# Optimization experiments

Measured on AMD Instinct MI355X. Metric: run time of the kernel, lower is better.

The kernel has to match this reference:

```python
import jax, jax.numpy as jnp
import numpy as np

B, N, M = 64, 128, 64
LH, LO, LI2, LI3, LI4 = 128, 128, 64, 32, 16


def _celu(x):
    return jax.nn.celu(x, alpha=0.1)


def setup_inputs() -> dict:
    key = jax.random.key(0)
    ks = jax.random.split(key, 32)
    inp = {
        'ai': jax.random.normal(ks[0], (B, N, 3), jnp.float32),
        'aj': jax.random.normal(ks[1], (B, N, M, 3), jnp.float32),
        'ak': jax.random.normal(ks[2], (B, N, M, 3), jnp.float32),
        'al': jax.random.normal(ks[3], (B, N, M, 3), jnp.float32),
    }
    def lin(k, fan_out, fan_in):
        kw, kb = jax.random.split(k)
        s = 1.0 / np.sqrt(fan_in)
        return (jax.random.uniform(kw, (fan_out, fan_in), jnp.float32, -s, s),
                jax.random.uniform(kb, (fan_out,), jnp.float32, -s, s))
    names = ['Wi1', 'Wi2', 'Wj1', 'Wj2', 'Wk1', 'Wk2', 'Wl1', 'Wl2']
    dims = [(LH, 3), (LO, LH)] * 4
    for i, (nm, (fo, fi)) in enumerate(zip(names, dims)):
        W, b = lin(ks[4 + i], fo, fi)
        inp[nm] = W
        inp['b' + nm[1:]] = b
    for i, (nm, (fo, fi)) in enumerate(zip(['W1', 'W2', 'W3', 'W4'],
                                           [(LI2, LO), (LI3, LI2), (LI4, LI3), (1, LI4)])):
        W, b = lin(ks[20 + i], fo, fi)
        inp[nm] = W
        inp['b' + nm[1:]] = b
    return inp


def _mlp2(x, W1, b1, W2, b2):
    return _celu(_celu(x @ W1.T + b1) @ W2.T + b2)


def _pad_mask(x):
    # 0 where the descriptor sums exactly to zero (padding), else 1
    s = x.sum(axis=-1)
    return (s != 0).astype(x.dtype)[..., None]


def reference(ai, aj, ak, al,
              Wi1, bi1, Wi2, bi2, Wj1, bj1, Wj2, bj2,
              Wk1, bk1, Wk2, bk2, Wl1, bl1, Wl2, bl2,
              W1, b1, W2, b2, W3, b3, W4, b4):
    ai_mask = _pad_mask(ai)          # [B,N,1]
    aj_mask = _pad_mask(aj)          # [B,N,M,1]
    ak_mask = _pad_mask(ak)
    al_mask = _pad_mask(al)

    hi = _mlp2(ai, Wi1, bi1, Wi2, bi2) * ai_mask            # [B,N,LO]
    hj = _mlp2(aj, Wj1, bj1, Wj2, bj2) * aj_mask            # [B,N,M,LO]
    hk = _mlp2(ak, Wk1, bk1, Wk2, bk2) * ak_mask
    hl = _mlp2(al, Wl1, bl1, Wl2, bl2) * al_mask

    atm = hi + hj.sum(axis=2) + hk.sum(axis=2) + hl.sum(axis=2)  # [B,N,LO]
    atm = _celu(atm @ W1.T + b1)
    atm = _celu(atm @ W2.T + b2)
    atm = _celu(atm @ W3.T + b3)
    atm = atm @ W4.T + b4                                    # [B,N,1]
    return atm * ai_mask
```

## Files before the change

### kernel.cpp

```cpp
#include <hip/hip_runtime.h>


typedef __attribute__((ext_vector_type(8))) short short8;
typedef __attribute__((ext_vector_type(4))) float f32x4;
typedef __attribute__((ext_vector_type(4))) unsigned uint4v;

#define G_ 8
#define NATOMS (64 * 128)
#define SCL   14.42695040888963f
#define SCL01 1.442695040888963f
#define INVS  0.06931471805599453f

#define LDS_BYTES 39712

struct DartParams {
  const float* x[4];
  const float* W1[4];
  const float* b1[4];
  const float* W2[4];
  const float* b2[4];
  const float* HW[4];
  const float* Hb[4];
  float* out;
};

__device__ __forceinline__ float celu01(float z) {
  float t = fmaf(0.1f, __builtin_amdgcn_exp2f(z * SCL), -0.1f);
  return __builtin_amdgcn_fmed3f(z, t, 0.0f);
}

__device__ __forceinline__ float celu_s(float zs) {
  float t = fmaf(SCL01, __builtin_amdgcn_exp2f(zs), -SCL01);
  return __builtin_amdgcn_fmed3f(zs, t, 0.0f);
}

__device__ __forceinline__ unsigned cvtpk(float a, float b) {
  unsigned r;
  asm("v_cvt_pk_bf16_f32 %0, %1, %2" : "=v"(r) : "v"(a), "v"(b));
  return r;
}
__device__ __forceinline__ short8 pack4(unsigned a, unsigned b, unsigned c, unsigned d) {
  uint4v u = {a, b, c, d};
  return __builtin_bit_cast(short8, u);
}

__device__ __forceinline__ void stage_species(
    const float* W1g, const float* b1g, const float* W2g, const float* b2g,
    f32x4* sW1v, float* sB2v, short8* sBfv,
    int t, int lane, int lq, int lr, int wave) {
  __syncthreads();
  if (t < 128) {
    const float* w = W1g + t * 3;
    f32x4 v;
    v.x = w[0] * SCL; v.y = w[1] * SCL; v.z = w[2] * SCL; v.w = b1g[t] * SCL;
    sW1v[t + (t >> 3)] = v;
    sB2v[t] = b2g[t] * SCL;
  }
#pragma unroll
  for (int ff = 0; ff < 8; ++ff) {
    const int f  = wave * 8 + ff;
    const int ob = f >> 2, kb = f & 3;
    const f32x4* src = (const f32x4*)(W2g + (ob * 16 + lr) * 128 + kb * 32 + lq * 8);
    f32x4 lo = src[0], hi = src[1];
    sBfv[f * 64 + lane] = pack4(cvtpk(lo.x, lo.y), cvtpk(lo.z, lo.w),
                                cvtpk(hi.x, hi.y), cvtpk(hi.z, hi.w));
  }
  __syncthreads();
}

extern "C" __global__ __launch_bounds__(256, 4)
void dart_fused(DartParams p) {
  __shared__ __align__(16) char lds[LDS_BYTES];
  short8* sBfv = (short8*)lds;
  f32x4*  sW1v = (f32x4*)(lds + 32768);
  float*  sB2v = (float*)(lds + 35072);
  float*  sAtm = (float*)(lds + 35584);
  float*  sIm  = (float*)(lds + 39680);
  float*  sH1  = (float*)lds;
  float*  sH2  = (float*)(lds + 2048);
  float*  sH3  = (float*)(lds + 3072);

  const int t    = threadIdx.x;
  const int lane = t & 63;
  const int wave = t >> 6;
  const int lq   = lane >> 4;
  const int lr   = lane & 15;
  const int atom0 = (int)blockIdx.x * G_;

  for (int i = t; i < G_ * 128; i += 256) sAtm[i] = 0.0f;

#pragma unroll 1
  for (int s = 0; s < 3; ++s) {
    stage_species(p.W1[s], p.b1[s], p.W2[s], p.b2[s],
                  sW1v, sB2v, sBfv, t, lane, lq, lr, wave);

    const float* X = p.x[s];
    const int rowoff = wave * 16 + lr;

#pragma unroll 1
    for (int qq = 0; qq < 2; ++qq) {
      const int gq = qq * 4;
      float x0[4], x1[4], x2[4];
#pragma unroll
      for (int a = 0; a < 4; ++a) {
        const float* xp = X + ((atom0 + gq + a) * 64 + rowoff) * 3;
        x0[a] = xp[0]; x1[a] = xp[1]; x2[a] = xp[2];
      }
      float mr[4][4];
#pragma unroll
      for (int a = 0; a < 4; ++a) {
        const unsigned mw = (unsigned)__ballot((x0[a] + x1[a] + x2[a]) != 0.0f);
#pragma unroll
        for (int j = 0; j < 4; ++j)
          mr[a][j] = ((mw >> (lq * 4 + j)) & 1u) ? INVS : 0.0f;
      }

      short8 af[4][4];
#pragma unroll
      for (int kb = 0; kb < 4; ++kb) {
        const f32x4* wrow = sW1v + kb * 36 + lq * 9;
        unsigned u[4][4];
#pragma unroll
        for (int e2 = 0; e2 < 4; ++e2) {
          f32x4 wA = wrow[2 * e2], wB = wrow[2 * e2 + 1];
#pragma unroll
          for (int a = 0; a < 4; ++a) {
            float zA = celu_s(fmaf(x0[a], wA.x, fmaf(x1[a], wA.y, fmaf(x2[a], wA.z, wA.w))));
            float zB = celu_s(fmaf(x0[a], wB.x, fmaf(x1[a], wB.y, fmaf(x2[a], wB.z, wB.w))));
            u[a][e2] = cvtpk(zA, zB);
          }
        }
#pragma unroll
        for (int a = 0; a < 4; ++a)
          af[a][kb] = pack4(u[a][0], u[a][1], u[a][2], u[a][3]);
      }

#pragma unroll
      for (int ob = 0; ob < 8; ++ob) {
        const short8* fb = sBfv + (ob * 4) * 64 + lane;
        const float bv = sB2v[ob * 16 + lr];
        f32x4 ac[4];
#pragma unroll
        for (int a = 0; a < 4; ++a) ac[a] = {bv, bv, bv, bv};
#pragma unroll
        for (int kb = 0; kb < 4; ++kb) {
          short8 fr = fb[kb * 64];
#pragma unroll
          for (int a = 0; a < 4; ++a)
            ac[a] = __builtin_amdgcn_mfma_f32_16x16x32_bf16(af[a][kb], fr, ac[a], 0, 0, 0);
        }
        const int col = ob * 16 + lr;
#pragma unroll
        for (int a = 0; a < 4; ++a) {
          float pa = 0.0f;
#pragma unroll
          for (int j = 0; j < 4; ++j)
            pa = fmaf(celu_s(ac[a][j]), mr[a][j], pa);
          pa += __shfl_xor(pa, 16, 64);
          pa += __shfl_xor(pa, 32, 64);
          if (lane < 16) atomicAdd(&sAtm[(gq + a) * 128 + col], pa);
        }
      }
    }
  }

  {
    stage_species(p.W1[3], p.b1[3], p.W2[3], p.b2[3],
                  sW1v, sB2v, sBfv, t, lane, lq, lr, wave);

    const int ri = min(atom0 + lr, NATOMS - 1);
    const float* xp = p.x[3] + ri * 3;
    const float x0 = xp[0], x1 = xp[1], x2 = xp[2];
    const unsigned mbi = (unsigned)__ballot((x0 + x1 + x2) != 0.0f);

    short8 af[4];
#pragma unroll
    for (int kb = 0; kb < 4; ++kb) {
      const f32x4* wrow = sW1v + kb * 36 + lq * 9;
      unsigned u[4];
#pragma unroll
      for (int e2 = 0; e2 < 4; ++e2) {
        f32x4 wA = wrow[2 * e2], wB = wrow[2 * e2 + 1];
        float cA = celu_s(fmaf(x0, wA.x, fmaf(x1, wA.y, fmaf(x2, wA.z, wA.w))));
        float cB = celu_s(fmaf(x0, wB.x, fmaf(x1, wB.y, fmaf(x2, wB.z, wB.w))));
        u[e2] = cvtpk(cA, cB);
      }
      af[kb] = pack4(u[0], u[1], u[2], u[3]);
    }
#pragma unroll
    for (int oo = 0; oo < 2; ++oo) {
      const int ob = wave * 2 + oo;
      const int col = ob * 16 + lr;
      const float bv = sB2v[col];
      const short8* fb = sBfv + (ob * 4) * 64 + lane;
      f32x4 a = {bv, bv, bv, bv};
#pragma unroll
      for (int kb = 0; kb < 4; ++kb)
        a = __builtin_amdgcn_mfma_f32_16x16x32_bf16(af[kb], fb[kb * 64], a, 0, 0, 0);
#pragma unroll
      for (int j = 0; j < 4; ++j) {
        const int g = lq * 4 + j;
        if (g < G_) {
          float m = ((mbi >> g) & 1u) ? INVS : 0.0f;
          sAtm[g * 128 + col] += celu_s(a[j]) * m;
        }
      }
    }
    if (wave == 0 && t < G_) sIm[t] = (float)((mbi >> t) & 1u);
    __syncthreads();
  }

  {
    const int g = t >> 4, u = t & 15;
    const bool act = (g < G_);
    if (act) {
      const f32x4* atm4 = (const f32x4*)(sAtm + g * 128);
#pragma unroll
      for (int rep = 0; rep < 4; ++rep) {
        const int o = rep * 16 + u;
        const f32x4* w4 = (const f32x4*)(p.HW[0] + o * 128);
        float z = p.Hb[0][o];
#pragma unroll 8
        for (int c = 0; c < 32; ++c) {
          f32x4 a = atm4[c], w = w4[c];
          z = fmaf(a.x, w.x, fmaf(a.y, w.y, fmaf(a.z, w.z, fmaf(a.w, w.w, z))));
        }
        sH1[g * 64 + o] = celu01(z);
      }
    }
    __syncthreads();
    if (act) {
      const f32x4* h14 = (const f32x4*)(sH1 + g * 64);
#pragma unroll
      for (int rep = 0; rep < 2; ++rep) {
        const int o = rep * 16 + u;
        const f32x4* w4 = (const f32x4*)(p.HW[1] + o * 64);
        float z = p.Hb[1][o];
#pragma unroll
        for (int c = 0; c < 16; ++c) {
          f32x4 a = h14[c], w = w4[c];
          z = fmaf(a.x, w.x, fmaf(a.y, w.y, fmaf(a.z, w.z, fmaf(a.w, w.w, z))));
        }
        sH2[g * 32 + o] = celu01(z);
      }
    }
    __syncthreads();
    if (act) {
      const f32x4* h24 = (const f32x4*)(sH2 + g * 32);
      const f32x4* w4 = (const f32x4*)(p.HW[2] + u * 32);
      float z = p.Hb[2][u];
#pragma unroll
      for (int c = 0; c < 8; ++c) {
        f32x4 a = h24[c], w = w4[c];
        z = fmaf(a.x, w.x, fmaf(a.y, w.y, fmaf(a.z, w.z, fmaf(a.w, w.w, z))));
      }
      sH3[g * 16 + u] = celu01(z);
    }
    __syncthreads();
    if (act && u == 0) {
      const f32x4* h34 = (const f32x4*)(sH3 + g * 16);
      const f32x4* w4 = (const f32x4*)p.HW[3];
      float z = p.Hb[3][0];
#pragma unroll
      for (int c = 0; c < 4; ++c) {
        f32x4 a = h34[c], w = w4[c];
        z = fmaf(a.x, w.x, fmaf(a.y, w.y, fmaf(a.z, w.z, fmaf(a.w, w.w, z))));
      }
      p.out[atom0 + g] = z * sIm[g];
    }
  }
}

extern "C" void kernel_launch(void* const* d_in, const int* in_sizes, int n_in,
                              void* d_out, int out_size, void* d_ws, size_t ws_size,
                              hipStream_t stream) {
  (void)in_sizes; (void)n_in; (void)out_size; (void)d_ws; (void)ws_size;
  DartParams p;
  p.x[0] = (const float*)d_in[1];
  p.x[1] = (const float*)d_in[2];
  p.x[2] = (const float*)d_in[3];
  p.x[3] = (const float*)d_in[0];
  p.W1[0] = (const float*)d_in[8];  p.b1[0] = (const float*)d_in[9];
  p.W2[0] = (const float*)d_in[10]; p.b2[0] = (const float*)d_in[11];
  p.W1[1] = (const float*)d_in[12]; p.b1[1] = (const float*)d_in[13];
  p.W2[1] = (const float*)d_in[14]; p.b2[1] = (const float*)d_in[15];
  p.W1[2] = (const float*)d_in[16]; p.b1[2] = (const float*)d_in[17];
  p.W2[2] = (const float*)d_in[18]; p.b2[2] = (const float*)d_in[19];
  p.W1[3] = (const float*)d_in[4];  p.b1[3] = (const float*)d_in[5];
  p.W2[3] = (const float*)d_in[6];  p.b2[3] = (const float*)d_in[7];
  p.HW[0] = (const float*)d_in[20]; p.Hb[0] = (const float*)d_in[21];
  p.HW[1] = (const float*)d_in[22]; p.Hb[1] = (const float*)d_in[23];
  p.HW[2] = (const float*)d_in[24]; p.Hb[2] = (const float*)d_in[25];
  p.HW[3] = (const float*)d_in[26]; p.Hb[3] = (const float*)d_in[27];
  p.out = (float*)d_out;

  dart_fused<<<dim3(NATOMS / G_), dim3(256), 0, stream>>>(p);
}
```

Before: 152.2 us.

## Precompute bf16 W2 fragments in a prep kernel and read from global

Adds a small prep kernel that converts all four species' W2 weights into bf16 MFMA fragment layout once, writing them to workspace. The main kernel then reads these fragments straight from global/L2 instead of every block re-converting W2 into shared memory, which cuts LDS use from about 39KB to about 10KB and removes per-block staging work. The cost is an extra launch and global loads inside the MFMA loop. The old LDS path is kept as a fallback when the workspace is too small.

Measured after the change: 215.0 us. 41.3% more time.

```diff
diff --git a/kernel.cpp b/kernel.cpp
--- a/kernel.cpp
+++ b/kernel.cpp
@@ -10,8 +10,7 @@
 #define SCL   14.42695040888963f
 #define SCL01 1.442695040888963f
 #define INVS  0.06931471805599453f
-
-#define LDS_BYTES 39712
+#define WS_BF_BYTES (4 * 32 * 64 * 16)
 
 struct DartParams {
   const float* x[4];
@@ -21,6 +20,7 @@
   const float* b2[4];
   const float* HW[4];
   const float* Hb[4];
+  const short8* gBf;
   float* out;
 };
 
@@ -28,12 +28,10 @@
   float t = fmaf(0.1f, __builtin_amdgcn_exp2f(z * SCL), -0.1f);
   return __builtin_amdgcn_fmed3f(z, t, 0.0f);
 }
-
 __device__ __forceinline__ float celu_s(float zs) {
   float t = fmaf(SCL01, __builtin_amdgcn_exp2f(zs), -SCL01);
   return __builtin_amdgcn_fmed3f(zs, t, 0.0f);
 }
-
 __device__ __forceinline__ unsigned cvtpk(float a, float b) {
   unsigned r;
   asm("v_cvt_pk_bf16_f32 %0, %1, %2" : "=v"(r) : "v"(a), "v"(b));
@@ -44,7 +42,246 @@
   return __builtin_bit_cast(short8, u);
 }
 
-__device__ __forceinline__ void stage_species(
+extern "C" __global__ __launch_bounds__(256)
+void dart_prep(const float* W2j, const float* W2k, const float* W2l,
+               const float* W2i, short8* ws) {
+  const int s = (int)blockIdx.x;
+  const float* W2 = (s == 0) ? W2j : (s == 1) ? W2k : (s == 2) ? W2l : W2i;
+  const int t = threadIdx.x;
+  const int lane = t & 63, wave = t >> 6;
+  const int lq = lane >> 4, lr = lane & 15;
+#pragma unroll
+  for (int ff = 0; ff < 8; ++ff) {
+    const int f  = wave * 8 + ff;
+    const int ob = f >> 2, kb = f & 3;
+    const f32x4* src = (const f32x4*)(W2 + (ob * 16 + lr) * 128 + kb * 32 + lq * 8);
+    f32x4 lo = src[0], hi = src[1];
+    ws[(s * 32 + f) * 64 + lane] = pack4(cvtpk(lo.x, lo.y), cvtpk(lo.z, lo.w),
+                                         cvtpk(hi.x, hi.y), cvtpk(hi.z, hi.w));
+  }
+}
+
+#define LDSG_BYTES 10528
+
+__device__ __forceinline__ void stage_w1(
+    const float* W1g, const float* b1g, const float* b2g,
+    f32x4* sW1v, float* sB2v, int t) {
+  __syncthreads();
+  if (t < 128) {
+    const float* w = W1g + t * 3;
+    f32x4 v;
+    v.x = w[0] * SCL; v.y = w[1] * SCL; v.z = w[2] * SCL; v.w = b1g[t] * SCL;
+    sW1v[t + (t >> 3)] = v;
+    sB2v[t] = b2g[t] * SCL;
+  }
+  __syncthreads();
+}
+
+extern "C" __global__ __launch_bounds__(256, 4)
+void dart_fused_g(DartParams p) {
+  __shared__ __align__(16) char lds[LDSG_BYTES];
+  f32x4*  sW1v = (f32x4*)lds;
+  float*  sB2v = (float*)(lds + 2304);
+  float*  sAtm = (float*)(lds + 2816);
+  float*  sIm  = (float*)(lds + 6912);
+  float*  sH1  = (float*)(lds + 6944);
+  float*  sH2  = (float*)(lds + 8992);
+  float*  sH3  = (float*)(lds + 10016);
+
+  const int t    = threadIdx.x;
+  const int lane = t & 63;
+  const int wave = t >> 6;
+  const int lq   = lane >> 4;
+  const int lr   = lane & 15;
+  const int atom0 = (int)blockIdx.x * G_;
+
+  for (int i = t; i < G_ * 128; i += 256) sAtm[i] = 0.0f;
+
+#pragma unroll 1
+  for (int s = 0; s < 3; ++s) {
+    stage_w1(p.W1[s], p.b1[s], p.b2[s], sW1v, sB2v, t);
+    const short8* gB = p.gBf + (s * 32) * 64 + lane;
+
+    const float* X = p.x[s];
+    const int rowoff = wave * 16 + lr;
+
+#pragma unroll 1
+    for (int qq = 0; qq < 2; ++qq) {
+      const int gq = qq * 4;
+      float x0[4], x1[4], x2[4];
+#pragma unroll
+      for (int a = 0; a < 4; ++a) {
+        const float* xp = X + ((atom0 + gq + a) * 64 + rowoff) * 3;
+        x0[a] = xp[0]; x1[a] = xp[1]; x2[a] = xp[2];
+      }
+      float mr[4][4];
+#pragma unroll
+      for (int a = 0; a < 4; ++a) {
+        const unsigned mw = (unsigned)__ballot((x0[a] + x1[a] + x2[a]) != 0.0f);
+#pragma unroll
+        for (int j = 0; j < 4; ++j)
+          mr[a][j] = ((mw >> (lq * 4 + j)) & 1u) ? INVS : 0.0f;
+      }
+
+      short8 af[4][4];
+#pragma unroll
+      for (int kb = 0; kb < 4; ++kb) {
+        const f32x4* wrow = sW1v + kb * 36 + lq * 9;
+        unsigned u[4][4];
+#pragma unroll
+        for (int e2 = 0; e2 < 4; ++e2) {
+          f32x4 wA = wrow[2 * e2], wB = wrow[2 * e2 + 1];
+#pragma unroll
+          for (int a = 0; a < 4; ++a) {
+            float zA = celu_s(fmaf(x0[a], wA.x, fmaf(x1[a], wA.y, fmaf(x2[a], wA.z, wA.w))));
+            float zB = celu_s(fmaf(x0[a], wB.x, fmaf(x1[a], wB.y, fmaf(x2[a], wB.z, wB.w))));
+            u[a][e2] = cvtpk(zA, zB);
+          }
+        }
+#pragma unroll
+        for (int a = 0; a < 4; ++a)
+          af[a][kb] = pack4(u[a][0], u[a][1], u[a][2], u[a][3]);
+      }
+
+#pragma unroll
+      for (int ob = 0; ob < 8; ++ob) {
+        const short8* fb = gB + (ob * 4) * 64;
+        const float bv = sB2v[ob * 16 + lr];
+        f32x4 ac[4];
+#pragma unroll
+        for (int a = 0; a < 4; ++a) ac[a] = {bv, bv, bv, bv};
+#pragma unroll
+        for (int kb = 0; kb < 4; ++kb) {
+          short8 fr = fb[kb * 64];
+#pragma unroll
+          for (int a = 0; a < 4; ++a)
+            ac[a] = __builtin_amdgcn_mfma_f32_16x16x32_bf16(af[a][kb], fr, ac[a], 0, 0, 0);
+        }
+        const int col = ob * 16 + lr;
+#pragma unroll
+        for (int a = 0; a < 4; ++a) {
+          float pa = 0.0f;
+#pragma unroll
+          for (int j = 0; j < 4; ++j)
+            pa = fmaf(celu_s(ac[a][j]), mr[a][j], pa);
+          pa += __shfl_xor(pa, 16, 64);
+          pa += __shfl_xor(pa, 32, 64);
+          if (lane < 16) atomicAdd(&sAtm[(gq + a) * 128 + col], pa);
+        }
+      }
+    }
+  }
+
+  {
+    stage_w1(p.W1[3], p.b1[3], p.b2[3], sW1v, sB2v, t);
+    const short8* gB = p.gBf + (3 * 32) * 64 + lane;
+
+    const int ri = min(atom0 + lr, NATOMS - 1);
+    const float* xp = p.x[3] + ri * 3;
+    const float x0 = xp[0], x1 = xp[1], x2 = xp[2];
+    const unsigned mbi = (unsigned)__ballot((x0 + x1 + x2) != 0.0f);
+
+    short8 af[4];
+#pragma unroll
+    for (int kb = 0; kb < 4; ++kb) {
+      const f32x4* wrow = sW1v + kb * 36 + lq * 9;
+      unsigned u[4];
+#pragma unroll
+      for (int e2 = 0; e2 < 4; ++e2) {
+        f32x4 wA = wrow[2 * e2], wB = wrow[2 * e2 + 1];
+        float cA = celu_s(fmaf(x0, wA.x, fmaf(x1, wA.y, fmaf(x2, wA.z, wA.w))));
+        float cB = celu_s(fmaf(x0, wB.x, fmaf(x1, wB.y, fmaf(x2, wB.z, wB.w))));
+        u[e2] = cvtpk(cA, cB);
+      }
+      af[kb] = pack4(u[0], u[1], u[2], u[3]);
+    }
+#pragma unroll
+    for (int oo = 0; oo < 2; ++oo) {
+      const int ob = wave * 2 + oo;
+      const int col = ob * 16 + lr;
+      const float bv = sB2v[col];
+      const short8* fb = gB + (ob * 4) * 64;
+      f32x4 a = {bv, bv, bv, bv};
+#pragma unroll
+      for (int kb = 0; kb < 4; ++kb)
+        a = __builtin_amdgcn_mfma_f32_16x16x32_bf16(af[kb], fb[kb * 64], a, 0, 0, 0);
+#pragma unroll
+      for (int j = 0; j < 4; ++j) {
+        const int g = lq * 4 + j;
+        if (g < G_) {
+          float m = ((mbi >> g) & 1u) ? INVS : 0.0f;
+          sAtm[g * 128 + col] += celu_s(a[j]) * m;
+        }
+      }
+    }
+    if (wave == 0 && t < G_) sIm[t] = (float)((mbi >> t) & 1u);
+    __syncthreads();
+  }
+
+  {
+    const int g = t >> 4, u = t & 15;
+    const bool act = (g < G_);
+    if (act) {
+      const f32x4* atm4 = (const f32x4*)(sAtm + g * 128);
+#pragma unroll
+      for (int rep = 0; rep < 4; ++rep) {
+        const int o = rep * 16 + u;
+        const f32x4* w4 = (const f32x4*)(p.HW[0] + o * 128);
+        float z = p.Hb[0][o];
+#pragma unroll 8
+        for (int c = 0; c < 32; ++c) {
+          f32x4 a = atm4[c], w = w4[c];
+          z = fmaf(a.x, w.x, fmaf(a.y, w.y, fmaf(a.z, w.z, fmaf(a.w, w.w, z))));
+        }
+        sH1[g * 64 + o] = celu01(z);
+      }
+    }
+    __syncthreads();
+    if (act) {
+      const f32x4* h14 = (const f32x4*)(sH1 + g * 64);
+#pragma unroll
+      for (int rep = 0; rep < 2; ++rep) {
+        const int o = rep * 16 + u;
+        const f32x4* w4 = (const f32x4*)(p.HW[1] + o * 64);
+        float z = p.Hb[1][o];
+#pragma unroll
+        for (int c = 0; c < 16; ++c) {
+          f32x4 a = h14[c], w = w4[c];
+          z = fmaf(a.x, w.x, fmaf(a.y, w.y, fmaf(a.z, w.z, fmaf(a.w, w.w, z))));
+        }
+        sH2[g * 32 + o] = celu01(z);
+      }
+    }
+    __syncthreads();
+    if (act) {
+      const f32x4* h24 = (const f32x4*)(sH2 + g * 32);
+      const f32x4* w4 = (const f32x4*)(p.HW[2] + u * 32);
+      float z = p.Hb[2][u];
+#pragma unroll
+      for (int c = 0; c < 8; ++c) {
+        f32x4 a = h24[c], w = w4[c];
+        z = fmaf(a.x, w.x, fmaf(a.y, w.y, fmaf(a.z, w.z, fmaf(a.w, w.w, z))));
+      }
+      sH3[g * 16 + u] = celu01(z);
+    }
+    __syncthreads();
+    if (act && u == 0) {
+      const f32x4* h34 = (const f32x4*)(sH3 + g * 16);
+      const f32x4* w4 = (const f32x4*)p.HW[3];
+      float z = p.Hb[3][0];
+#pragma unroll
+      for (int c = 0; c < 4; ++c) {
+        f32x4 a = h34[c], w = w4[c];
+        z = fmaf(a.x, w.x, fmaf(a.y, w.y, fmaf(a.z, w.z, fmaf(a.w, w.w, z))));
+      }
+      p.out[atom0 + g] = z * sIm[g];
+    }
+  }
+}
+
+#define LDS_BYTES 39712
+
+__device__ __forceinline__ void stage_species_l(
     const float* W1g, const float* b1g, const float* W2g, const float* b2g,
     f32x4* sW1v, float* sB2v, short8* sBfv,
     int t, int lane, int lq, int lr, int wave) {
@@ -69,7 +306,7 @@
 }
 
 extern "C" __global__ __launch_bounds__(256, 4)
-void dart_fused(DartParams p) {
+void dart_fused_l(DartParams p) {
   __shared__ __align__(16) char lds[LDS_BYTES];
   short8* sBfv = (short8*)lds;
   f32x4*  sW1v = (f32x4*)(lds + 32768);
@@ -91,12 +328,10 @@
 
 #pragma unroll 1
   for (int s = 0; s < 3; ++s) {
-    stage_species(p.W1[s], p.b1[s], p.W2[s], p.b2[s],
-                  sW1v, sB2v, sBfv, t, lane, lq, lr, wave);
-
+    stage_species_l(p.W1[s], p.b1[s], p.W2[s], p.b2[s],
+                    sW1v, sB2v, sBfv, t, lane, lq, lr, wave);
     const float* X = p.x[s];
     const int rowoff = wave * 16 + lr;
-
 #pragma unroll 1
     for (int qq = 0; qq < 2; ++qq) {
       const int gq = qq * 4;
@@ -114,7 +349,6 @@
         for (int j = 0; j < 4; ++j)
           mr[a][j] = ((mw >> (lq * 4 + j)) & 1u) ? INVS : 0.0f;
       }
-
       short8 af[4][4];
 #pragma unroll
       for (int kb = 0; kb < 4; ++kb) {
@@ -134,7 +368,6 @@
         for (int a = 0; a < 4; ++a)
           af[a][kb] = pack4(u[a][0], u[a][1], u[a][2], u[a][3]);
       }
-
 #pragma unroll
       for (int ob = 0; ob < 8; ++ob) {
         const short8* fb = sBfv + (ob * 4) * 64 + lane;
@@ -163,16 +396,13 @@
       }
     }
   }
-
   {
-    stage_species(p.W1[3], p.b1[3], p.W2[3], p.b2[3],
-                  sW1v, sB2v, sBfv, t, lane, lq, lr, wave);
-
+    stage_species_l(p.W1[3], p.b1[3], p.W2[3], p.b2[3],
+                    sW1v, sB2v, sBfv, t, lane, lq, lr, wave);
     const int ri = min(atom0 + lr, NATOMS - 1);
     const float* xp = p.x[3] + ri * 3;
     const float x0 = xp[0], x1 = xp[1], x2 = xp[2];
     const unsigned mbi = (unsigned)__ballot((x0 + x1 + x2) != 0.0f);
-
     short8 af[4];
 #pragma unroll
     for (int kb = 0; kb < 4; ++kb) {
@@ -209,7 +439,6 @@
     if (wave == 0 && t < G_) sIm[t] = (float)((mbi >> t) & 1u);
     __syncthreads();
   }
-
   {
     const int g = t >> 4, u = t & 15;
     const bool act = (g < G_);
@@ -274,7 +503,7 @@
 extern "C" void kernel_launch(void* const* d_in, const int* in_sizes, int n_in,
                               void* d_out, int out_size, void* d_ws, size_t ws_size,
                               hipStream_t stream) {
-  (void)in_sizes; (void)n_in; (void)out_size; (void)d_ws; (void)ws_size;
+  (void)in_sizes; (void)n_in; (void)out_size;
   DartParams p;
   p.x[0] = (const float*)d_in[1];
   p.x[1] = (const float*)d_in[2];
@@ -294,5 +523,13 @@
   p.HW[3] = (const float*)d_in[26]; p.Hb[3] = (const float*)d_in[27];
   p.out = (float*)d_out;
 
-  dart_fused<<<dim3(NATOMS / G_), dim3(256), 0, stream>>>(p);
-}
+  if (ws_size >= (size_t)WS_BF_BYTES) {
+    short8* ws = (short8*)d_ws;
+    p.gBf = ws;
+    dart_prep<<<dim3(4), dim3(256), 0, stream>>>(p.W2[0], p.W2[1], p.W2[2], p.W2[3], ws);
+    dart_fused_g<<<dim3(NATOMS / G_), dim3(256), 0, stream>>>(p);
+  } else {
+    p.gBf = nullptr;
+    dart_fused_l<<<dim3(NATOMS / G_), dim3(256), 0, stream>>>(p);
+  }
+}
```
